# Kernel tuning notes

Measured on AMD Instinct MI355X. Metric: run time of the kernel, lower is better.

## Reference

```python
import jax, jax.numpy as jnp
import numpy as np

# norse LIFParameters defaults
SEQ_LENGTH = 100
DT = 1e-3
TAU_MEM_INV = 100.0  # 1 / 1e-2
V_LEAK = 0.0
V_TH = 1.0
V_RESET = 0.0
ALPHA = 100.0  # SuperSpike surrogate sharpness ('super' method)


@jax.custom_vjp
def heaviside(x):
    # Forward: hard threshold; backward: SuperSpike surrogate (defined below).
    return (x > 0).astype(x.dtype)


def _heaviside_fwd(x):
    return (x > 0).astype(x.dtype), x


def _heaviside_bwd(x, g):
    # SuperSpike: d/dx ~ 1 / (alpha*|x| + 1)^2
    sg = 1.0 / (ALPHA * jnp.abs(x) + 1.0) ** 2
    return (g * sg,)


heaviside.defvjp(_heaviside_fwd, _heaviside_bwd)


def setup_inputs() -> dict:
    key = jax.random.key(0)
    # Constant input currents in [0, 2): mix of sub- and supra-threshold neurons.
    input_currents = jax.random.uniform(key, (32, 8192), dtype=jnp.float32) * 2.0
    return {"input_currents": input_currents}


def reference(input_currents):
    """constant_current_lif_encode: simulate SEQ_LENGTH LIF steps with a
    constant input current; return spike trains [seq_length, *input.shape]."""

    def step(v, _):
        dv = DT * TAU_MEM_INV * ((V_LEAK - v) + input_currents)
        v = v + dv
        z = heaviside(v - V_TH)
        v = v - z * (v - V_RESET)  # reset-to-V_RESET on spike
        return v, z

    v0 = jnp.zeros_like(input_currents)
    _, spikes = jax.lax.scan(step, v0, None, length=SEQ_LENGTH)
    return spikes  # [SEQ_LENGTH, batch, n_neurons]
```

## Files before the change

kernel.cpp:

```cpp
#include <hip/hip_runtime.h>


#define LIF_SEQ_LENGTH 100

__global__ __launch_bounds__(256)
void ConstantCurrentLIFEncoder_10436770530031_kernel(
    const float* __restrict__ in, float* __restrict__ out, int n)
{
    const int i = blockIdx.x * blockDim.x + threadIdx.x;
    if (i >= n) return;

    const float I = in[i];
    float v = 0.0f;

    #pragma unroll
    for (int t = 0; t < LIF_SEQ_LENGTH; ++t) {
        v = __fadd_rn(v, __fmul_rn(0.1f, __fsub_rn(I, v)));

        const bool spike = (v > 1.0f);
        out[(size_t)t * (size_t)n + (size_t)i] = spike ? 1.0f : 0.0f;
        if (spike) v = 0.0f;
    }
}

extern "C" void kernel_launch(void* const* d_in, const int* in_sizes, int n_in,
                              void* d_out, int out_size, void* d_ws, size_t ws_size,
                              hipStream_t stream) {
    const float* in = (const float*)d_in[0];
    float* out = (float*)d_out;
    const int n = in_sizes[0];
    const int block = 256;
    const int grid = (n + block - 1) / block;
    ConstantCurrentLIFEncoder_10436770530031_kernel<<<grid, block, 0, stream>>>(in, out, n);
}
```

Baseline: 22.11 us.

## Split time steps into quarters across threads with float4 vectorized stores

Each thread now handles four neurons through float4 loads and stores, and the 100 time steps are split into four 25-step chunks assigned to different threads. Each thread recomputes the membrane state for the earlier chunks without writing output, so the grid size stays the same while writes become 128-bit and per-thread work is spread more evenly. The indexing hardcodes n4 = 65536 (tid>>16, mask n4-1), so it only works when n4 is a power of two equal to 2^16. It also adds redundant recompute for later chunks, which unbalances work across threads.

Result: no change. 22.26 us (+0.6%).

```diff
diff --git a/kernel.cpp b/kernel.cpp
--- a/kernel.cpp
+++ b/kernel.cpp
@@ -1,25 +1,55 @@
 #include <hip/hip_runtime.h>
 
 
-#define LIF_SEQ_LENGTH 100
+#define QSTEPS 25
 
 __global__ __launch_bounds__(256)
 void ConstantCurrentLIFEncoder_10436770530031_kernel(
-    const float* __restrict__ in, float* __restrict__ out, int n)
+    const float* __restrict__ in, float* __restrict__ out, int n4)
 {
-    const int i = blockIdx.x * blockDim.x + threadIdx.x;
-    if (i >= n) return;
+    const int tid = blockIdx.x * blockDim.x + threadIdx.x;
+    const int i = tid & (n4 - 1);
+    const int q = tid >> 16;
 
-    const float I = in[i];
-    float v = 0.0f;
+    const float4 I = reinterpret_cast<const float4*>(in)[i];
+    float4* __restrict__ out4 = reinterpret_cast<float4*>(out);
+
+    float v0 = 0.0f, v1 = 0.0f, v2 = 0.0f, v3 = 0.0f;
+
+    for (int tq = 0; tq < q; ++tq) {
+        #pragma unroll
+        for (int t = 0; t < QSTEPS; ++t) {
+            v0 = __fadd_rn(v0, __fmul_rn(0.1f, __fsub_rn(I.x, v0)));
+            v1 = __fadd_rn(v1, __fmul_rn(0.1f, __fsub_rn(I.y, v1)));
+            v2 = __fadd_rn(v2, __fmul_rn(0.1f, __fsub_rn(I.z, v2)));
+            v3 = __fadd_rn(v3, __fmul_rn(0.1f, __fsub_rn(I.w, v3)));
+            if (v0 > 1.0f) v0 = 0.0f;
+            if (v1 > 1.0f) v1 = 0.0f;
+            if (v2 > 1.0f) v2 = 0.0f;
+            if (v3 > 1.0f) v3 = 0.0f;
+        }
+    }
+
+    float4* __restrict__ o = out4 + (size_t)q * QSTEPS * (size_t)n4 + (size_t)i;
 
     #pragma unroll
-    for (int t = 0; t < LIF_SEQ_LENGTH; ++t) {
-        v = __fadd_rn(v, __fmul_rn(0.1f, __fsub_rn(I, v)));
+    for (int t = 0; t < QSTEPS; ++t) {
+        v0 = __fadd_rn(v0, __fmul_rn(0.1f, __fsub_rn(I.x, v0)));
+        v1 = __fadd_rn(v1, __fmul_rn(0.1f, __fsub_rn(I.y, v1)));
+        v2 = __fadd_rn(v2, __fmul_rn(0.1f, __fsub_rn(I.z, v2)));
+        v3 = __fadd_rn(v3, __fmul_rn(0.1f, __fsub_rn(I.w, v3)));
 
-        const bool spike = (v > 1.0f);
-        out[(size_t)t * (size_t)n + (size_t)i] = spike ? 1.0f : 0.0f;
-        if (spike) v = 0.0f;
+        float4 z;
+        z.x = (v0 > 1.0f) ? 1.0f : 0.0f;
+        z.y = (v1 > 1.0f) ? 1.0f : 0.0f;
+        z.z = (v2 > 1.0f) ? 1.0f : 0.0f;
+        z.w = (v3 > 1.0f) ? 1.0f : 0.0f;
+        o[(size_t)t * (size_t)n4] = z;
+
+        if (z.x != 0.0f) v0 = 0.0f;
+        if (z.y != 0.0f) v1 = 0.0f;
+        if (z.z != 0.0f) v2 = 0.0f;
+        if (z.w != 0.0f) v3 = 0.0f;
     }
 }
 
@@ -29,7 +59,8 @@
     const float* in = (const float*)d_in[0];
     float* out = (float*)d_out;
     const int n = in_sizes[0];
+    const int n4 = n / 4;
     const int block = 256;
-    const int grid = (n + block - 1) / block;
-    ConstantCurrentLIFEncoder_10436770530031_kernel<<<grid, block, 0, stream>>>(in, out, n);
+    const int grid = (4 * n4) / block;
+    ConstantCurrentLIFEncoder_10436770530031_kernel<<<grid, block, 0, stream>>>(in, out, n4);
 }
```
